# Performance work log

Measured on AMD Instinct MI355X. Metric: run time of the kernel, lower is better.

The kernel has to match this reference:

```python
import jax, jax.numpy as jnp
import numpy as np
import math

B, N, F_IN, F_OUT = 16, 2048, 256, 64


def setup_inputs() -> dict:
    key = jax.random.key(0)
    k1, k2, k3, k4 = jax.random.split(key, 4)
    x = jax.random.normal(k1, (B, N, F_IN), dtype=jnp.float32)
    adj = jax.random.randint(k2, (B, N, N), 0, 2, dtype=jnp.int32)
    stdv = 1.0 / math.sqrt(F_OUT)
    weight = jax.random.uniform(k3, (F_IN, F_OUT), dtype=jnp.float32, minval=-stdv, maxval=stdv)
    # weight2 stdv = 1/sqrt(1) = 1.0
    weight2 = jax.random.uniform(k4, (2 * F_OUT, 1), dtype=jnp.float32, minval=-1.0, maxval=1.0)
    return {"x": x, "adj": adj, "weight": weight, "weight2": weight2}


def reference(x, adj, weight, weight2):
    # h[b,n,o] = (x @ weight)  -- shared linear projection
    h = jnp.einsum("bni,io->bno", x, weight)
    Fo = weight.shape[1]
    # Split additive-attention vector: e_ij = relu(h_i . a_src + h_j . a_dst)
    # Mathematically identical to cat([h_i, h_j]) @ weight2 of the original.
    a_src = weight2[:Fo, 0]
    a_dst = weight2[Fo:, 0]
    s_src = jnp.einsum("bno,o->bn", h, a_src)  # [B, N]
    s_dst = jnp.einsum("bno,o->bn", h, a_dst)  # [B, N]
    e = jax.nn.relu(s_src[:, :, None] + s_dst[:, None, :])  # [B, N, N]
    NEG = jnp.float32(-9e15)
    scores = jnp.where(adj > 0, e, NEG)
    attention = jax.nn.softmax(scores, axis=2)  # softmax over neighbors j
    # dropout = 0.0 / eval mode -> identity
    out = jnp.einsum("bij,bjo->bio", attention, h)  # [B, N, F_OUT]
    return out
```

## Files before the change

kernel.cpp:

```cpp
#include <hip/hip_runtime.h>
#include <hip/hip_bf16.h>

#define BB 16
#define NN 2048
#define FIN 256
#define FO 64
#define CH 256
#define HSTR 264

typedef __bf16 bf16x8 __attribute__((ext_vector_type(8)));
typedef float  f32x4  __attribute__((ext_vector_type(4)));
typedef int    i32x4  __attribute__((ext_vector_type(4)));
typedef unsigned int uint;
typedef unsigned short ushort;

__global__ __launch_bounds__(256) void k_pack(const int* __restrict__ adj,
                                              ushort* __restrict__ mask) {
    size_t t = (size_t)blockIdx.x * 256 + threadIdx.x;
    const i32x4* ap = (const i32x4*)(adj + t * 16);
    i32x4 a0 = ap[0], a1 = ap[1], a2 = ap[2], a3 = ap[3];
    uint b = (uint)(a0.x > 0) | ((uint)(a0.y > 0) << 1) |
             ((uint)(a0.z > 0) << 2) | ((uint)(a0.w > 0) << 3) |
             ((uint)(a1.x > 0) << 4) | ((uint)(a1.y > 0) << 5) |
             ((uint)(a1.z > 0) << 6) | ((uint)(a1.w > 0) << 7) |
             ((uint)(a2.x > 0) << 8) | ((uint)(a2.y > 0) << 9) |
             ((uint)(a2.z > 0) << 10) | ((uint)(a2.w > 0) << 11) |
             ((uint)(a3.x > 0) << 12) | ((uint)(a3.y > 0) << 13) |
             ((uint)(a3.z > 0) << 14) | ((uint)(a3.w > 0) << 15);
    mask[t] = (ushort)b;
}

__global__ __launch_bounds__(256) void k1_gemm(
    const float* __restrict__ x, const float* __restrict__ weight,
    const float* __restrict__ w2,
    __bf16* __restrict__ hT, float* __restrict__ s_src, float* __restrict__ s_dst) {
    __shared__ __bf16 WtL[FO * 264];
    __shared__ float vsL[FIN], vdL[FIN];
    int t = threadIdx.x;
    {
        const float4* wr = (const float4*)(weight + t * FO);
        float a = 0.f, d = 0.f;
#pragma unroll
        for (int c = 0; c < 16; ++c) {
            float4 v = wr[c];
            int o = c * 4;
            WtL[(o + 0) * 264 + t] = (__bf16)v.x;
            WtL[(o + 1) * 264 + t] = (__bf16)v.y;
            WtL[(o + 2) * 264 + t] = (__bf16)v.z;
            WtL[(o + 3) * 264 + t] = (__bf16)v.w;
            a += v.x * w2[o] + v.y * w2[o + 1] + v.z * w2[o + 2] + v.w * w2[o + 3];
            d += v.x * w2[FO + o] + v.y * w2[FO + o + 1] +
                 v.z * w2[FO + o + 2] + v.w * w2[FO + o + 3];
        }
        vsL[t] = a;
        vdL[t] = d;
    }
    __syncthreads();

    int lane = threadIdx.x & 63, w = threadIdx.x >> 6;
    int quad = lane >> 4, m = lane & 15;
    int Rbase = blockIdx.x * 64 + w * 16;
    int R = Rbase + m;
    const float* xr = x + (long)R * FIN;

    f32x4 acc[4] = {};
    float ps = 0.f, pd = 0.f;

#pragma unroll
    for (int k0 = 0; k0 < FIN; k0 += 32) {
        int kb = k0 + quad * 8;
        float4 x0 = *(const float4*)(xr + kb);
        float4 x1 = *(const float4*)(xr + kb + 4);
        float4 u0 = *(const float4*)(vsL + kb);
        float4 u1 = *(const float4*)(vsL + kb + 4);
        float4 t0 = *(const float4*)(vdL + kb);
        float4 t1 = *(const float4*)(vdL + kb + 4);
        ps += x0.x * u0.x + x0.y * u0.y + x0.z * u0.z + x0.w * u0.w +
              x1.x * u1.x + x1.y * u1.y + x1.z * u1.z + x1.w * u1.w;
        pd += x0.x * t0.x + x0.y * t0.y + x0.z * t0.z + x0.w * t0.w +
              x1.x * t1.x + x1.y * t1.y + x1.z * t1.z + x1.w * t1.w;
        bf16x8 bf = {(__bf16)x0.x, (__bf16)x0.y, (__bf16)x0.z, (__bf16)x0.w,
                     (__bf16)x1.x, (__bf16)x1.y, (__bf16)x1.z, (__bf16)x1.w};
#pragma unroll
        for (int ot = 0; ot < 4; ++ot) {
            bf16x8 af = *(const bf16x8*)(WtL + (ot * 16 + m) * 264 + kb);
            acc[ot] = __builtin_amdgcn_mfma_f32_16x16x32_bf16(af, bf, acc[ot], 0, 0, 0);
        }
    }
    ps += __shfl_xor(ps, 16);
    ps += __shfl_xor(ps, 32);
    pd += __shfl_xor(pd, 16);
    pd += __shfl_xor(pd, 32);
    if (quad == 0) {
        s_src[R] = ps;
        s_dst[R] = pd;
    }
    int b = R >> 11;
    int nb = Rbase & (NN - 1);
#pragma unroll
    for (int ot = 0; ot < 4; ++ot) {
#pragma unroll
        for (int r = 0; r < 4; ++r) {
            int o = ot * 16 + quad * 4 + r;
            hT[((long)b * FO + o) * NN + nb + m] = (__bf16)acc[ot][r];
        }
    }
}

__global__ __launch_bounds__(256, 4) void k2_attn(
    const unsigned char* __restrict__ mask, const float* __restrict__ s_src,
    const float* __restrict__ s_dst, const __bf16* __restrict__ hT,
    float* __restrict__ out) {
    __shared__ __bf16 hL[FO * HSTR];
    __shared__ float EL[NN];
    int b = blockIdx.x >> 5;
    int i0 = (blockIdx.x & 31) << 6;
    int lane = threadIdx.x & 63, w = threadIdx.x >> 6;
    int quad = lane >> 4, m = lane & 15;
    int rowbase = i0 + w * 16;
    int row = rowbase + m;

    const float* sd = s_dst + b * NN;
    float mx = -3.0e38f;
    for (int j = lane; j < NN; j += 64) mx = fmaxf(mx, sd[j]);
#pragma unroll
    for (int off = 32; off >= 1; off >>= 1) mx = fmaxf(mx, __shfl_xor(mx, off));
    {
        int j0 = threadIdx.x * 8;
        float4 v0 = *(const float4*)(sd + j0);
        float4 v1 = *(const float4*)(sd + j0 + 4);
        EL[j0 + 0] = __expf(v0.x - mx);
        EL[j0 + 1] = __expf(v0.y - mx);
        EL[j0 + 2] = __expf(v0.z - mx);
        EL[j0 + 3] = __expf(v0.w - mx);
        EL[j0 + 4] = __expf(v1.x - mx);
        EL[j0 + 5] = __expf(v1.y - mx);
        EL[j0 + 6] = __expf(v1.z - mx);
        EL[j0 + 7] = __expf(v1.w - mx);
    }

    float T = s_src[b * NN + row] + mx;
    float cK = __expf(-T);

    const uint4* mrow = (const uint4*)(mask + ((size_t)(b * NN + row)) * 256);
    int q8 = quad * 8;
    int so = threadIdx.x >> 2;
    int sseg = (threadIdx.x & 3) * 64;

    f32x4 acc[4] = {};
    f32x4 accL = {};
    const bf16x8 ones = {(__bf16)1.f, (__bf16)1.f, (__bf16)1.f, (__bf16)1.f,
                         (__bf16)1.f, (__bf16)1.f, (__bf16)1.f, (__bf16)1.f};

    for (int c = 0; c < NN / CH; ++c) {
        __syncthreads();
        {
            const bf16x8* src =
                (const bf16x8*)(hT + ((long)b * FO + so) * NN + c * CH + sseg);
            bf16x8* dst = (bf16x8*)(hL + so * HSTR + sseg);
            bf16x8 v0 = src[0], v1 = src[1], v2 = src[2], v3 = src[3];
            bf16x8 v4 = src[4], v5 = src[5], v6 = src[6], v7 = src[7];
            dst[0] = v0; dst[1] = v1; dst[2] = v2; dst[3] = v3;
            dst[4] = v4; dst[5] = v5; dst[6] = v6; dst[7] = v7;
        }
        __syncthreads();
        uint4 mv0 = mrow[c * 2], mv1 = mrow[c * 2 + 1];
        uint mg[8] = {mv0.x, mv0.y, mv0.z, mv0.w, mv1.x, mv1.y, mv1.z, mv1.w};
#pragma unroll
        for (int u = 0; u < 8; ++u) {
            int ksg = c * 8 + u;
            uint mb = (mg[u] >> q8) & 0xffu;
            const float* ep = EL + ksg * 32 + q8;
            float4 e0 = *(const float4*)ep;
            float4 e1 = *(const float4*)(ep + 4);
            float p0 = (mb & 1u)   ? fmaxf(e0.x, cK) : 0.f;
            float p1 = (mb & 2u)   ? fmaxf(e0.y, cK) : 0.f;
            float p2 = (mb & 4u)   ? fmaxf(e0.z, cK) : 0.f;
            float p3 = (mb & 8u)   ? fmaxf(e0.w, cK) : 0.f;
            float p4 = (mb & 16u)  ? fmaxf(e1.x, cK) : 0.f;
            float p5 = (mb & 32u)  ? fmaxf(e1.y, cK) : 0.f;
            float p6 = (mb & 64u)  ? fmaxf(e1.z, cK) : 0.f;
            float p7 = (mb & 128u) ? fmaxf(e1.w, cK) : 0.f;
            bf16x8 af = {(__bf16)p0, (__bf16)p1, (__bf16)p2, (__bf16)p3,
                         (__bf16)p4, (__bf16)p5, (__bf16)p6, (__bf16)p7};
            accL = __builtin_amdgcn_mfma_f32_16x16x32_bf16(af, ones, accL, 0, 0, 0);
            const __bf16* hb = hL + u * 32 + q8;
#pragma unroll
            for (int ot = 0; ot < 4; ++ot) {
                bf16x8 bf = *(const bf16x8*)(hb + (ot * 16 + m) * HSTR);
                acc[ot] = __builtin_amdgcn_mfma_f32_16x16x32_bf16(af, bf, acc[ot], 0, 0, 0);
            }
        }
    }

    float* outp = out + ((long)b * NN + rowbase) * FO;
#pragma unroll
    for (int r = 0; r < 4; ++r) {
        int orow = quad * 4 + r;
        float inv = 1.0f / accL[r];
#pragma unroll
        for (int ot = 0; ot < 4; ++ot) {
            outp[(long)orow * FO + ot * 16 + m] = acc[ot][r] * inv;
        }
    }
}

extern "C" void kernel_launch(void* const* d_in, const int* in_sizes, int n_in,
                              void* d_out, int out_size, void* d_ws, size_t ws_size,
                              hipStream_t stream) {
    const float* x      = (const float*)d_in[0];
    const int*   adj    = (const int*)d_in[1];
    const float* weight = (const float*)d_in[2];
    const float* w2     = (const float*)d_in[3];
    float* out = (float*)d_out;

    char* ws = (char*)d_ws;
    __bf16* hT   = (__bf16*)ws;
    float* s_src = (float*)(ws + 4194304);
    float* s_dst = (float*)(ws + 4194304 + 131072);
    unsigned char* mask = (unsigned char*)(ws + 4194304 + 262144);

    k_pack<<<16384, 256, 0, stream>>>(adj, (ushort*)mask);
    k1_gemm<<<512, 256, 0, stream>>>(x, weight, w2, hT, s_src, s_dst);
    k2_attn<<<512, 256, 0, stream>>>(mask, s_src, s_dst, hT, out);
}
```

Measured before the change: 424.0 us.

## Prefetch next hT chunk and mask into registers; nontemporal byte-wise adj packing

The attention kernel now loads the next 256-column chunk of hT and the next mask words into registers while computing on the current chunk, so global-load latency overlaps with the MFMA work. The launch-bounds occupancy hint drops from 4 to 2 blocks per CU to leave room for the extra staging registers. The pack kernel now has each thread read 8 ints with nontemporal loads and write one byte, using twice as many threads. The extra registers lower occupancy, and this could offset the latency hiding.

```diff
diff --git a/kernel.cpp b/kernel.cpp
--- a/kernel.cpp
+++ b/kernel.cpp
@@ -12,22 +12,18 @@
 typedef float  f32x4  __attribute__((ext_vector_type(4)));
 typedef int    i32x4  __attribute__((ext_vector_type(4)));
 typedef unsigned int uint;
-typedef unsigned short ushort;
 
 __global__ __launch_bounds__(256) void k_pack(const int* __restrict__ adj,
-                                              ushort* __restrict__ mask) {
+                                              unsigned char* __restrict__ mask) {
     size_t t = (size_t)blockIdx.x * 256 + threadIdx.x;
-    const i32x4* ap = (const i32x4*)(adj + t * 16);
-    i32x4 a0 = ap[0], a1 = ap[1], a2 = ap[2], a3 = ap[3];
-    uint b = (uint)(a0.x > 0) | ((uint)(a0.y > 0) << 1) |
-             ((uint)(a0.z > 0) << 2) | ((uint)(a0.w > 0) << 3) |
-             ((uint)(a1.x > 0) << 4) | ((uint)(a1.y > 0) << 5) |
-             ((uint)(a1.z > 0) << 6) | ((uint)(a1.w > 0) << 7) |
-             ((uint)(a2.x > 0) << 8) | ((uint)(a2.y > 0) << 9) |
-             ((uint)(a2.z > 0) << 10) | ((uint)(a2.w > 0) << 11) |
-             ((uint)(a3.x > 0) << 12) | ((uint)(a3.y > 0) << 13) |
-             ((uint)(a3.z > 0) << 14) | ((uint)(a3.w > 0) << 15);
-    mask[t] = (ushort)b;
+    const i32x4* ap = (const i32x4*)(adj + t * 8);
+    i32x4 a0 = __builtin_nontemporal_load(ap);
+    i32x4 a1 = __builtin_nontemporal_load(ap + 1);
+    unsigned b = (unsigned)(a0.x > 0) | ((unsigned)(a0.y > 0) << 1) |
+                 ((unsigned)(a0.z > 0) << 2) | ((unsigned)(a0.w > 0) << 3) |
+                 ((unsigned)(a1.x > 0) << 4) | ((unsigned)(a1.y > 0) << 5) |
+                 ((unsigned)(a1.z > 0) << 6) | ((unsigned)(a1.w > 0) << 7);
+    mask[t] = (unsigned char)b;
 }
 
 __global__ __launch_bounds__(256) void k1_gemm(
@@ -107,7 +103,7 @@
     }
 }
 
-__global__ __launch_bounds__(256, 4) void k2_attn(
+__global__ __launch_bounds__(256, 2) void k2_attn(
     const unsigned char* __restrict__ mask, const float* __restrict__ s_src,
     const float* __restrict__ s_dst, const __bf16* __restrict__ hT,
     float* __restrict__ out) {
@@ -142,10 +138,21 @@
     float T = s_src[b * NN + row] + mx;
     float cK = __expf(-T);
 
+    int so = threadIdx.x >> 2;
+    int sc = (threadIdx.x & 3) * 64;
+    const __bf16* hsrc = hT + ((long)b * FO + so) * NN + sc;
+    __bf16* hdst = hL + so * HSTR + sc;
+
     const uint4* mrow = (const uint4*)(mask + ((size_t)(b * NN + row)) * 256);
     int q8 = quad * 8;
-    int so = threadIdx.x >> 2;
-    int sseg = (threadIdx.x & 3) * 64;
+
+    bf16x8 st[8];
+    {
+        const bf16x8* sp = (const bf16x8*)hsrc;
+#pragma unroll
+        for (int i = 0; i < 8; ++i) st[i] = sp[i];
+    }
+    uint4 mv0 = mrow[0], mv1 = mrow[1];
 
     f32x4 acc[4] = {};
     f32x4 accL = {};
@@ -155,17 +162,19 @@
     for (int c = 0; c < NN / CH; ++c) {
         __syncthreads();
         {
-            const bf16x8* src =
-                (const bf16x8*)(hT + ((long)b * FO + so) * NN + c * CH + sseg);
-            bf16x8* dst = (bf16x8*)(hL + so * HSTR + sseg);
-            bf16x8 v0 = src[0], v1 = src[1], v2 = src[2], v3 = src[3];
-            bf16x8 v4 = src[4], v5 = src[5], v6 = src[6], v7 = src[7];
-            dst[0] = v0; dst[1] = v1; dst[2] = v2; dst[3] = v3;
-            dst[4] = v4; dst[5] = v5; dst[6] = v6; dst[7] = v7;
+            bf16x8* dp = (bf16x8*)hdst;
+#pragma unroll
+            for (int i = 0; i < 8; ++i) dp[i] = st[i];
         }
         __syncthreads();
-        uint4 mv0 = mrow[c * 2], mv1 = mrow[c * 2 + 1];
         uint mg[8] = {mv0.x, mv0.y, mv0.z, mv0.w, mv1.x, mv1.y, mv1.z, mv1.w};
+        if (c < NN / CH - 1) {
+            const bf16x8* sp = (const bf16x8*)(hsrc + (c + 1) * CH);
+#pragma unroll
+            for (int i = 0; i < 8; ++i) st[i] = sp[i];
+            mv0 = mrow[(c + 1) * 2];
+            mv1 = mrow[(c + 1) * 2 + 1];
+        }
 #pragma unroll
         for (int u = 0; u < 8; ++u) {
             int ksg = c * 8 + u;
@@ -220,7 +229,7 @@
     float* s_dst = (float*)(ws + 4194304 + 131072);
     unsigned char* mask = (unsigned char*)(ws + 4194304 + 262144);
 
-    k_pack<<<16384, 256, 0, stream>>>(adj, (ushort*)mask);
+    k_pack<<<32768, 256, 0, stream>>>(adj, mask);
     k1_gemm<<<512, 256, 0, stream>>>(x, weight, w2, hT, s_src, s_dst);
     k2_attn<<<512, 256, 0, stream>>>(mask, s_src, s_dst, hT, out);
 }
```

Measured after the change: 408.0 us. 3.8% less time.
